# Optimization experiments

Hardware: AMD Instinct MI355X
Metric: run time of the kernel (lower is better)

The kernel has to match this reference:

```python
import jax, jax.numpy as jnp
import numpy as np

U, I, D, K, B, NNEG = 500000, 500000, 64, 32, 8192, 128
W1, W2, W3, W4 = 1e-6, 1.0, 1e-6, 1.0
NEG_WEIGHT, GAMMA, LAMBDA = 200.0, 1e-4, 2.5


def setup_inputs() -> dict:
    key = jax.random.key(0)
    ks = jax.random.split(key, 14)
    return {
        "users": jax.random.randint(ks[0], (B,), 0, U),
        "pos_items": jax.random.randint(ks[1], (B,), 0, I),
        "neg_items": jax.random.randint(ks[2], (B, NNEG), 0, I),
        "rpkms": jax.random.normal(ks[3], (B,), dtype=jnp.float32),
        "user_emb": jax.random.normal(ks[4], (U, D), dtype=jnp.float32) * 1e-2,
        "item_emb": jax.random.normal(ks[5], (I, D), dtype=jnp.float32) * 1e-2,
        "beta_uD": jax.random.uniform(ks[6], (U,), dtype=jnp.float32),
        "beta_iD": jax.random.uniform(ks[7], (I,), dtype=jnp.float32),
        "ii_neighbor_mat": jax.random.randint(ks[8], (I, K), 0, I),
        "ii_constraint_mat": jax.random.uniform(ks[9], (I, K), dtype=jnp.float32),
        "mse_u_w": jax.random.normal(ks[10], (D, D), dtype=jnp.float32) * 0.05,
        "mse_u_b": jnp.zeros((D,), jnp.float32),
        "mse_i_w": jax.random.normal(ks[11], (D, D), dtype=jnp.float32) * 0.05,
        "mse_i_b": jnp.zeros((D,), jnp.float32),
        "fc1_w1": jax.random.normal(ks[12], (D, 2 * D), dtype=jnp.float32) * 0.05,
        "fc1_b1": jnp.zeros((D,), jnp.float32),
        "fc1_w2": jax.random.normal(ks[13], (1, D), dtype=jnp.float32) * 0.05,
        "fc1_b2": jnp.zeros((1,), jnp.float32),
    }


def reference(users, pos_items, neg_items, rpkms, user_emb, item_emb,
              beta_uD, beta_iD, ii_neighbor_mat, ii_constraint_mat,
              mse_u_w, mse_u_b, mse_i_w, mse_i_b,
              fc1_w1, fc1_b1, fc1_w2, fc1_b2):
    sp = jax.nn.softplus  # -log(sigmoid(x)) == softplus(-x)

    ue = user_emb[users]            # [B, D]
    pe = item_emb[pos_items]        # [B, D]
    ne = item_emb[neg_items]        # [B, N, D]

    # ---- omegas ----
    pos_w = W1 + W2 * beta_uD[users] * beta_iD[pos_items]          # [B]
    neg_w = W3 + W4 * beta_uD[users][:, None] * beta_iD[neg_items]  # [B, N]

    # ---- cal_loss_L (weighted BCE with logits) ----
    pos_scores = jnp.sum(ue * pe, axis=-1)                  # [B]
    neg_scores = jnp.einsum('bd,bnd->bn', ue, ne)           # [B, N]
    pos_loss = pos_w * sp(-pos_scores)                      # label 1
    neg_loss = jnp.mean(neg_w * sp(neg_scores), axis=-1)    # label 0, mean over negs
    loss_L = jnp.mean(pos_loss + neg_loss * NEG_WEIGHT)

    # ---- norm_loss over all learned parameters ----
    params = (user_emb, item_emb, mse_u_w, mse_u_b, mse_i_w, mse_i_b,
              fc1_w1, fc1_b1, fc1_w2, fc1_b2)
    norm = GAMMA * 0.5 * sum(jnp.sum(p * p) for p in params)

    # ---- cal_loss_I: gather item-item neighbors of pos_items ----
    nbr = item_emb[ii_neighbor_mat[pos_items]]              # [B, K, D]
    sim = ii_constraint_mat[pos_items]                      # [B, K]
    loss_I = LAMBDA * jnp.mean(sim * sp(-jnp.einsum('bd,bkd->bk', ue, nbr)))

    # ---- mse_loss ----
    feat_u = ue @ mse_u_w.T + mse_u_b
    feat_i = pe @ mse_i_w.T + mse_i_b
    pred = jnp.sum(feat_u * feat_i, axis=-1)
    mse = jnp.mean((pred - rpkms) ** 2)

    total = loss_L + norm + loss_I + mse
    zero = jnp.float32(0.0)  # torch returns torch.tensor(0.0) as 4th element
    return jnp.stack([total, loss_L, loss_I, zero, mse, norm])
```

## Files before the change

kernel.cpp:

```cpp
#include <hip/hip_runtime.h>
#include <math.h>

#define UU 500000
#define II 500000
#define DD 64
#define KK 32
#define BB 8192
#define NNEG 128

__device__ __forceinline__ float softplus_f(float x) {
    return fmaxf(x, 0.0f) + log1pf(expf(-fabsf(x)));
}

__device__ __forceinline__ float waveReduceSum(float v) {
#pragma unroll
    for (int off = 32; off > 0; off >>= 1) v += __shfl_xor(v, off, 64);
    return v;
}

__global__ __launch_bounds__(256) void fused_kernel(
    const int* __restrict__ users, const int* __restrict__ pos_items,
    const int* __restrict__ neg_items,
    const float* __restrict__ user_emb, const float* __restrict__ item_emb,
    const float* __restrict__ beta_uD, const float* __restrict__ beta_iD,
    const int* __restrict__ ii_nbr, const float* __restrict__ ii_con,
    const float* __restrict__ mse_u_w, const float* __restrict__ mse_u_b,
    const float* __restrict__ mse_i_w, const float* __restrict__ mse_i_b,
    const float* __restrict__ fc1_w1, const float* __restrict__ fc1_b1,
    const float* __restrict__ fc1_w2, const float* __restrict__ fc1_b2,
    float* __restrict__ acc)
{
    float norm_s = 0.f, accL = 0.f, accI = 0.f;

    {
        const size_t tid    = (size_t)blockIdx.x * blockDim.x + threadIdx.x;
        const size_t stride = (size_t)gridDim.x * blockDim.x;
        const size_t n4 = (size_t)UU * DD / 4;
        const float4* a = (const float4*)user_emb;
        for (size_t i = tid; i < n4; i += stride) {
            float4 v = a[i];
            norm_s += v.x * v.x + v.y * v.y + v.z * v.z + v.w * v.w;
        }
        const float4* c = (const float4*)item_emb;
        for (size_t i = tid; i < n4; i += stride) {
            float4 v = c[i];
            norm_s += v.x * v.x + v.y * v.y + v.z * v.z + v.w * v.w;
        }
        for (size_t i = tid; i < (size_t)DD * DD; i += stride)
            norm_s += mse_u_w[i] * mse_u_w[i] + mse_i_w[i] * mse_i_w[i];
        for (size_t i = tid; i < (size_t)DD * 2 * DD; i += stride)
            norm_s += fc1_w1[i] * fc1_w1[i];
        for (size_t i = tid; i < (size_t)DD; i += stride)
            norm_s += mse_u_b[i] * mse_u_b[i] + mse_i_b[i] * mse_i_b[i]
                    + fc1_b1[i] * fc1_b1[i] + fc1_w2[i] * fc1_w2[i];
        if (tid == 0) norm_s += fc1_b2[0] * fc1_b2[0];
    }

    const int wave = threadIdx.x >> 6;
    const int lane = threadIdx.x & 63;
    const int b = blockIdx.x * 4 + wave;

    const int u_idx = users[b];
    const int p_idx = pos_items[b];
    const float u_reg = user_emb[(size_t)u_idx * DD + lane];
    const float bu = beta_uD[u_idx];

    {
        const float p = item_emb[(size_t)p_idx * DD + lane];
        const float pos_dot = waveReduceSum(u_reg * p);
        if (lane == 0)
            accL += (1e-6f + bu * beta_iD[p_idx]) * softplus_f(-pos_dot);
    }

    const int i0 = neg_items[(size_t)b * NNEG + lane];
    const int i1 = neg_items[(size_t)b * NNEG + 64 + lane];
    const float bn0 = beta_iD[i0];
    const float bn1 = beta_iD[i1];

    const int q  = lane & 3;
    const int li = lane >> 2;
    const float negscale4 = 0.25f * (200.0f / (float)NNEG);

#pragma unroll 2
    for (int p = 0; p < 8; ++p) {
        const int n = p * 16 + li;
        int idx; float bi;
        if (p < 4) { idx = __shfl(i0, n, 64);      bi = __shfl(bn0, n, 64); }
        else       { idx = __shfl(i1, n - 64, 64); bi = __shfl(bn1, n - 64, 64); }
        const float* row = item_emb + (size_t)idx * DD;
        float dot = 0.f;
#pragma unroll
        for (int j = 0; j < 4; ++j) {
            const float4 v = *(const float4*)(row + j * 16 + q * 4);
            const int base = j * 16 + q * 4;
            dot = fmaf(v.x, __shfl(u_reg, base + 0, 64), dot);
            dot = fmaf(v.y, __shfl(u_reg, base + 1, 64), dot);
            dot = fmaf(v.z, __shfl(u_reg, base + 2, 64), dot);
            dot = fmaf(v.w, __shfl(u_reg, base + 3, 64), dot);
        }
        dot += __shfl_xor(dot, 1, 64);
        dot += __shfl_xor(dot, 2, 64);
        accL += negscale4 * (1e-6f + bu * bi) * softplus_f(dot);
    }

    int nbv = 0; float simv = 0.f;
    if (lane < KK) {
        nbv  = ii_nbr[(size_t)p_idx * KK + lane];
        simv = ii_con[(size_t)p_idx * KK + lane];
    }
#pragma unroll
    for (int p = 0; p < 2; ++p) {
        const int n = p * 16 + li;
        const int idx  = __shfl(nbv, n, 64);
        const float sk = __shfl(simv, n, 64);
        const float* row = item_emb + (size_t)idx * DD;
        float dot = 0.f;
#pragma unroll
        for (int j = 0; j < 4; ++j) {
            const float4 v = *(const float4*)(row + j * 16 + q * 4);
            const int base = j * 16 + q * 4;
            dot = fmaf(v.x, __shfl(u_reg, base + 0, 64), dot);
            dot = fmaf(v.y, __shfl(u_reg, base + 1, 64), dot);
            dot = fmaf(v.z, __shfl(u_reg, base + 2, 64), dot);
            dot = fmaf(v.w, __shfl(u_reg, base + 3, 64), dot);
        }
        dot += __shfl_xor(dot, 1, 64);
        dot += __shfl_xor(dot, 2, 64);
        accI += 0.25f * sk * softplus_f(-dot);
    }

    norm_s = waveReduceSum(norm_s);
    accL   = waveReduceSum(accL);
    accI   = waveReduceSum(accI);
    __shared__ float red[3][4];
    if (lane == 0) { red[0][wave] = norm_s; red[1][wave] = accL; red[2][wave] = accI; }
    __syncthreads();
    if (threadIdx.x == 0) {
        atomicAdd(&acc[0], red[1][0] + red[1][1] + red[1][2] + red[1][3]);
        atomicAdd(&acc[1], red[2][0] + red[2][1] + red[2][2] + red[2][3]);
        atomicAdd(&acc[2], red[0][0] + red[0][1] + red[0][2] + red[0][3]);
    }
}

__global__ __launch_bounds__(256) void mse_kernel(
    const int* __restrict__ users, const int* __restrict__ pos_items,
    const float* __restrict__ rpkms,
    const float* __restrict__ user_emb, const float* __restrict__ item_emb,
    const float* __restrict__ mse_u_w, const float* __restrict__ mse_u_b,
    const float* __restrict__ mse_i_w, const float* __restrict__ mse_i_b,
    float* __restrict__ acc)
{
    __shared__ float sWu[DD * (DD + 1)];
    __shared__ float sWi[DD * (DD + 1)];
    __shared__ float sBu[DD], sBi[DD];
    __shared__ float sUe[4][DD], sPe[4][DD];

    for (int i = threadIdx.x; i < DD * DD; i += blockDim.x) {
        const int r = i >> 6, c = i & 63;
        sWu[r * (DD + 1) + c] = mse_u_w[i];
        sWi[r * (DD + 1) + c] = mse_i_w[i];
    }
    if (threadIdx.x < DD) {
        sBu[threadIdx.x] = mse_u_b[threadIdx.x];
        sBi[threadIdx.x] = mse_i_b[threadIdx.x];
    }

    const int wave = threadIdx.x >> 6;
    const int lane = threadIdx.x & 63;
    const int b = blockIdx.x * 4 + wave;
    sUe[wave][lane] = user_emb[(size_t)users[b] * DD + lane];
    sPe[wave][lane] = item_emb[(size_t)pos_items[b] * DD + lane];
    __syncthreads();

    float fu = sBu[lane];
    float fi = sBi[lane];
#pragma unroll 8
    for (int d = 0; d < DD; ++d) {
        fu += sUe[wave][d] * sWu[lane * (DD + 1) + d];
        fi += sPe[wave][d] * sWi[lane * (DD + 1) + d];
    }
    const float pred = waveReduceSum(fu * fi);
    if (lane == 0) {
        const float diff = pred - rpkms[b];
        atomicAdd(&acc[3], diff * diff);
    }
}

__global__ void finalize_kernel(const float* __restrict__ acc, float* __restrict__ out)
{
    if (threadIdx.x == 0) {
        const float loss_L = acc[0] / (float)BB;
        const float loss_I = 2.5f * acc[1] / (float)(BB * KK);
        const float mse    = acc[3] / (float)BB;
        const float norm   = 1e-4f * 0.5f * acc[2];
        const float total  = loss_L + norm + loss_I + mse;
        out[0] = total;
        out[1] = loss_L;
        out[2] = loss_I;
        out[3] = 0.0f;
        out[4] = mse;
        out[5] = norm;
    }
}

extern "C" void kernel_launch(void* const* d_in, const int* in_sizes, int n_in,
                              void* d_out, int out_size, void* d_ws, size_t ws_size,
                              hipStream_t stream)
{
    const int*   users      = (const int*)  d_in[0];
    const int*   pos_items  = (const int*)  d_in[1];
    const int*   neg_items  = (const int*)  d_in[2];
    const float* rpkms      = (const float*)d_in[3];
    const float* user_emb   = (const float*)d_in[4];
    const float* item_emb   = (const float*)d_in[5];
    const float* beta_uD    = (const float*)d_in[6];
    const float* beta_iD    = (const float*)d_in[7];
    const int*   ii_nbr     = (const int*)  d_in[8];
    const float* ii_con     = (const float*)d_in[9];
    const float* mse_u_w    = (const float*)d_in[10];
    const float* mse_u_b    = (const float*)d_in[11];
    const float* mse_i_w    = (const float*)d_in[12];
    const float* mse_i_b    = (const float*)d_in[13];
    const float* fc1_w1     = (const float*)d_in[14];
    const float* fc1_b1     = (const float*)d_in[15];
    const float* fc1_w2     = (const float*)d_in[16];
    const float* fc1_b2     = (const float*)d_in[17];

    float* acc = (float*)d_ws;
    hipMemsetAsync(d_ws, 0, 4 * sizeof(float), stream);

    fused_kernel<<<BB / 4, 256, 0, stream>>>(users, pos_items, neg_items,
                                             user_emb, item_emb, beta_uD, beta_iD,
                                             ii_nbr, ii_con,
                                             mse_u_w, mse_u_b, mse_i_w, mse_i_b,
                                             fc1_w1, fc1_b1, fc1_w2, fc1_b2, acc);

    mse_kernel<<<BB / 4, 256, 0, stream>>>(users, pos_items, rpkms,
                                           user_emb, item_emb,
                                           mse_u_w, mse_u_b, mse_i_w, mse_i_b, acc);

    finalize_kernel<<<1, 64, 0, stream>>>(acc, (float*)d_out);
}
```

Before: 554.7 us.

## Split norm reduction into dedicated blocks and batch gather loads with LDS user vector

Gives the full-table norm reduction its own 1024 blocks, separate from the gather blocks, so the streaming sweep no longer sits in front of the gather work in every block. The sweep is unrolled four ways with independent accumulators, and the user-embedding pass uses nontemporal loads. In the gather path the user vector is staged through LDS into registers instead of being broadcast with shuffles per element, and all rows of a group are loaded before any are consumed, to raise memory-level parallelism. The cost is more registers and a larger grid, plus possible contention between the streaming and gather blocks.

```diff
diff --git a/kernel.cpp b/kernel.cpp
--- a/kernel.cpp
+++ b/kernel.cpp
@@ -7,6 +7,11 @@
 #define KK 32
 #define BB 8192
 #define NNEG 128
+
+#define NORMB 1024
+#define GATHB (BB / 4)
+
+typedef float v4f __attribute__((ext_vector_type(4)));
 
 __device__ __forceinline__ float softplus_f(float x) {
     return fmaxf(x, 0.0f) + log1pf(expf(-fabsf(x)));
@@ -30,40 +35,88 @@
     const float* __restrict__ fc1_w2, const float* __restrict__ fc1_b2,
     float* __restrict__ acc)
 {
-    float norm_s = 0.f, accL = 0.f, accI = 0.f;
-
-    {
-        const size_t tid    = (size_t)blockIdx.x * blockDim.x + threadIdx.x;
-        const size_t stride = (size_t)gridDim.x * blockDim.x;
-        const size_t n4 = (size_t)UU * DD / 4;
-        const float4* a = (const float4*)user_emb;
-        for (size_t i = tid; i < n4; i += stride) {
-            float4 v = a[i];
-            norm_s += v.x * v.x + v.y * v.y + v.z * v.z + v.w * v.w;
-        }
-        const float4* c = (const float4*)item_emb;
-        for (size_t i = tid; i < n4; i += stride) {
-            float4 v = c[i];
-            norm_s += v.x * v.x + v.y * v.y + v.z * v.z + v.w * v.w;
-        }
-        for (size_t i = tid; i < (size_t)DD * DD; i += stride)
-            norm_s += mse_u_w[i] * mse_u_w[i] + mse_i_w[i] * mse_i_w[i];
-        for (size_t i = tid; i < (size_t)DD * 2 * DD; i += stride)
-            norm_s += fc1_w1[i] * fc1_w1[i];
-        for (size_t i = tid; i < (size_t)DD; i += stride)
-            norm_s += mse_u_b[i] * mse_u_b[i] + mse_i_b[i] * mse_i_b[i]
-                    + fc1_b1[i] * fc1_b1[i] + fc1_w2[i] * fc1_w2[i];
-        if (tid == 0) norm_s += fc1_b2[0] * fc1_b2[0];
-    }
-
     const int wave = threadIdx.x >> 6;
     const int lane = threadIdx.x & 63;
-    const int b = blockIdx.x * 4 + wave;
+    __shared__ float red[4];
+
+    if (blockIdx.x < NORMB) {
+        const size_t tid = (size_t)blockIdx.x * blockDim.x + threadIdx.x;
+        const size_t st  = (size_t)NORMB * 256;
+        const size_t n4  = (size_t)UU * DD / 4;
+        float s0 = 0.f, s1 = 0.f, s2 = 0.f, s3 = 0.f;
+
+        {
+            const v4f* a = (const v4f*)user_emb;
+            size_t i = tid;
+            for (; i + 3 * st < n4; i += 4 * st) {
+                v4f x0 = __builtin_nontemporal_load(&a[i]);
+                v4f x1 = __builtin_nontemporal_load(&a[i + st]);
+                v4f x2 = __builtin_nontemporal_load(&a[i + 2 * st]);
+                v4f x3 = __builtin_nontemporal_load(&a[i + 3 * st]);
+                s0 += x0.x*x0.x + x0.y*x0.y + x0.z*x0.z + x0.w*x0.w;
+                s1 += x1.x*x1.x + x1.y*x1.y + x1.z*x1.z + x1.w*x1.w;
+                s2 += x2.x*x2.x + x2.y*x2.y + x2.z*x2.z + x2.w*x2.w;
+                s3 += x3.x*x3.x + x3.y*x3.y + x3.z*x3.z + x3.w*x3.w;
+            }
+            for (; i < n4; i += st) {
+                v4f x = __builtin_nontemporal_load(&a[i]);
+                s0 += x.x*x.x + x.y*x.y + x.z*x.z + x.w*x.w;
+            }
+        }
+        {
+            const v4f* c = (const v4f*)item_emb;
+            size_t i = tid;
+            for (; i + 3 * st < n4; i += 4 * st) {
+                v4f x0 = c[i];
+                v4f x1 = c[i + st];
+                v4f x2 = c[i + 2 * st];
+                v4f x3 = c[i + 3 * st];
+                s0 += x0.x*x0.x + x0.y*x0.y + x0.z*x0.z + x0.w*x0.w;
+                s1 += x1.x*x1.x + x1.y*x1.y + x1.z*x1.z + x1.w*x1.w;
+                s2 += x2.x*x2.x + x2.y*x2.y + x2.z*x2.z + x2.w*x2.w;
+                s3 += x3.x*x3.x + x3.y*x3.y + x3.z*x3.z + x3.w*x3.w;
+            }
+            for (; i < n4; i += st) {
+                v4f x = c[i];
+                s0 += x.x*x.x + x.y*x.y + x.z*x.z + x.w*x.w;
+            }
+        }
+        float s = (s0 + s1) + (s2 + s3);
+        for (size_t i = tid; i < (size_t)DD * DD; i += st)
+            s += mse_u_w[i] * mse_u_w[i] + mse_i_w[i] * mse_i_w[i];
+        for (size_t i = tid; i < (size_t)DD * 2 * DD; i += st)
+            s += fc1_w1[i] * fc1_w1[i];
+        for (size_t i = tid; i < (size_t)DD; i += st)
+            s += mse_u_b[i] * mse_u_b[i] + mse_i_b[i] * mse_i_b[i]
+               + fc1_b1[i] * fc1_b1[i] + fc1_w2[i] * fc1_w2[i];
+        if (tid == 0) s += fc1_b2[0] * fc1_b2[0];
+
+        s = waveReduceSum(s);
+        if (lane == 0) red[wave] = s;
+        __syncthreads();
+        if (threadIdx.x == 0)
+            atomicAdd(&acc[2], red[0] + red[1] + red[2] + red[3]);
+        return;
+    }
+
+    const int b = (blockIdx.x - NORMB) * 4 + wave;
+    float accL = 0.f, accI = 0.f;
 
     const int u_idx = users[b];
     const int p_idx = pos_items[b];
     const float u_reg = user_emb[(size_t)u_idx * DD + lane];
     const float bu = beta_uD[u_idx];
+
+    __shared__ float sU[4][DD];
+    sU[wave][lane] = u_reg;
+
+    const int q  = lane & 3;
+    const int li = lane >> 2;
+
+    float4 uv[4];
+#pragma unroll
+    for (int j = 0; j < 4; ++j)
+        uv[j] = *(const float4*)&sU[wave][j * 16 + q * 4];
 
     {
         const float p = item_emb[(size_t)p_idx * DD + lane];
@@ -77,30 +130,38 @@
     const float bn0 = beta_iD[i0];
     const float bn1 = beta_iD[i1];
 
-    const int q  = lane & 3;
-    const int li = lane >> 2;
     const float negscale4 = 0.25f * (200.0f / (float)NNEG);
 
-#pragma unroll 2
-    for (int p = 0; p < 8; ++p) {
-        const int n = p * 16 + li;
-        int idx; float bi;
-        if (p < 4) { idx = __shfl(i0, n, 64);      bi = __shfl(bn0, n, 64); }
-        else       { idx = __shfl(i1, n - 64, 64); bi = __shfl(bn1, n - 64, 64); }
-        const float* row = item_emb + (size_t)idx * DD;
-        float dot = 0.f;
-#pragma unroll
-        for (int j = 0; j < 4; ++j) {
-            const float4 v = *(const float4*)(row + j * 16 + q * 4);
-            const int base = j * 16 + q * 4;
-            dot = fmaf(v.x, __shfl(u_reg, base + 0, 64), dot);
-            dot = fmaf(v.y, __shfl(u_reg, base + 1, 64), dot);
-            dot = fmaf(v.z, __shfl(u_reg, base + 2, 64), dot);
-            dot = fmaf(v.w, __shfl(u_reg, base + 3, 64), dot);
-        }
-        dot += __shfl_xor(dot, 1, 64);
-        dot += __shfl_xor(dot, 2, 64);
-        accL += negscale4 * (1e-6f + bu * bi) * softplus_f(dot);
+#pragma unroll
+    for (int g = 0; g < 2; ++g) {
+        const int   srcI = g ? i1 : i0;
+        const float srcB = g ? bn1 : bn0;
+        float4 vb[4][4];
+        float  bi4[4];
+#pragma unroll
+        for (int t = 0; t < 4; ++t) {
+            const int n = t * 16 + li;
+            const int idx = __shfl(srcI, n, 64);
+            bi4[t] = __shfl(srcB, n, 64);
+            const float* row = item_emb + (size_t)idx * DD + q * 4;
+#pragma unroll
+            for (int j = 0; j < 4; ++j)
+                vb[t][j] = *(const float4*)(row + j * 16);
+        }
+#pragma unroll
+        for (int t = 0; t < 4; ++t) {
+            float dot = 0.f;
+#pragma unroll
+            for (int j = 0; j < 4; ++j) {
+                dot = fmaf(vb[t][j].x, uv[j].x, dot);
+                dot = fmaf(vb[t][j].y, uv[j].y, dot);
+                dot = fmaf(vb[t][j].z, uv[j].z, dot);
+                dot = fmaf(vb[t][j].w, uv[j].w, dot);
+            }
+            dot += __shfl_xor(dot, 1, 64);
+            dot += __shfl_xor(dot, 2, 64);
+            accL += negscale4 * (1e-6f + bu * bi4[t]) * softplus_f(dot);
+        }
     }
 
     int nbv = 0; float simv = 0.f;
@@ -108,37 +169,43 @@
         nbv  = ii_nbr[(size_t)p_idx * KK + lane];
         simv = ii_con[(size_t)p_idx * KK + lane];
     }
-#pragma unroll
-    for (int p = 0; p < 2; ++p) {
-        const int n = p * 16 + li;
-        const int idx  = __shfl(nbv, n, 64);
-        const float sk = __shfl(simv, n, 64);
-        const float* row = item_emb + (size_t)idx * DD;
-        float dot = 0.f;
-#pragma unroll
-        for (int j = 0; j < 4; ++j) {
-            const float4 v = *(const float4*)(row + j * 16 + q * 4);
-            const int base = j * 16 + q * 4;
-            dot = fmaf(v.x, __shfl(u_reg, base + 0, 64), dot);
-            dot = fmaf(v.y, __shfl(u_reg, base + 1, 64), dot);
-            dot = fmaf(v.z, __shfl(u_reg, base + 2, 64), dot);
-            dot = fmaf(v.w, __shfl(u_reg, base + 3, 64), dot);
-        }
-        dot += __shfl_xor(dot, 1, 64);
-        dot += __shfl_xor(dot, 2, 64);
-        accI += 0.25f * sk * softplus_f(-dot);
-    }
-
-    norm_s = waveReduceSum(norm_s);
-    accL   = waveReduceSum(accL);
-    accI   = waveReduceSum(accI);
-    __shared__ float red[3][4];
-    if (lane == 0) { red[0][wave] = norm_s; red[1][wave] = accL; red[2][wave] = accI; }
+    {
+        float4 vb[2][4];
+        float  sk2[2];
+#pragma unroll
+        for (int t = 0; t < 2; ++t) {
+            const int n = t * 16 + li;
+            const int idx = __shfl(nbv, n, 64);
+            sk2[t] = __shfl(simv, n, 64);
+            const float* row = item_emb + (size_t)idx * DD + q * 4;
+#pragma unroll
+            for (int j = 0; j < 4; ++j)
+                vb[t][j] = *(const float4*)(row + j * 16);
+        }
+#pragma unroll
+        for (int t = 0; t < 2; ++t) {
+            float dot = 0.f;
+#pragma unroll
+            for (int j = 0; j < 4; ++j) {
+                dot = fmaf(vb[t][j].x, uv[j].x, dot);
+                dot = fmaf(vb[t][j].y, uv[j].y, dot);
+                dot = fmaf(vb[t][j].z, uv[j].z, dot);
+                dot = fmaf(vb[t][j].w, uv[j].w, dot);
+            }
+            dot += __shfl_xor(dot, 1, 64);
+            dot += __shfl_xor(dot, 2, 64);
+            accI += 0.25f * sk2[t] * softplus_f(-dot);
+        }
+    }
+
+    accL = waveReduceSum(accL);
+    accI = waveReduceSum(accI);
+    __shared__ float redL[4], redI[4];
+    if (lane == 0) { redL[wave] = accL; redI[wave] = accI; }
     __syncthreads();
     if (threadIdx.x == 0) {
-        atomicAdd(&acc[0], red[1][0] + red[1][1] + red[1][2] + red[1][3]);
-        atomicAdd(&acc[1], red[2][0] + red[2][1] + red[2][2] + red[2][3]);
-        atomicAdd(&acc[2], red[0][0] + red[0][1] + red[0][2] + red[0][3]);
+        atomicAdd(&acc[0], redL[0] + redL[1] + redL[2] + redL[3]);
+        atomicAdd(&acc[1], redI[0] + redI[1] + redI[2] + redI[3]);
     }
 }
 
@@ -229,11 +296,11 @@
     float* acc = (float*)d_ws;
     hipMemsetAsync(d_ws, 0, 4 * sizeof(float), stream);
 
-    fused_kernel<<<BB / 4, 256, 0, stream>>>(users, pos_items, neg_items,
-                                             user_emb, item_emb, beta_uD, beta_iD,
-                                             ii_nbr, ii_con,
-                                             mse_u_w, mse_u_b, mse_i_w, mse_i_b,
-                                             fc1_w1, fc1_b1, fc1_w2, fc1_b2, acc);
+    fused_kernel<<<NORMB + GATHB, 256, 0, stream>>>(users, pos_items, neg_items,
+                                                    user_emb, item_emb, beta_uD, beta_iD,
+                                                    ii_nbr, ii_con,
+                                                    mse_u_w, mse_u_b, mse_i_w, mse_i_b,
+                                                    fc1_w1, fc1_b1, fc1_w2, fc1_b2, acc);
 
     mse_kernel<<<BB / 4, 256, 0, stream>>>(users, pos_items, rpkms,
                                            user_emb, item_emb,
```

New measurement: 531.5 us. -4.2%, faster.
